# Kernel optimization log

Hardware: AMD Instinct MI355X
Metric: run time of the kernel (lower is better)

Reference implementation:

```python
import jax, jax.numpy as jnp
import numpy as np

VOCAB, EMB, HID, OUT = 32000, 512, 1024, 2
B, T = 64, 512


def setup_inputs() -> dict:
    key = jax.random.key(0)
    ks = jax.random.split(key, 12)
    def xavier(k, shape):
        fan_in, fan_out = shape
        lim = np.sqrt(6.0 / (fan_in + fan_out)).astype(np.float32)
        return jax.random.uniform(k, shape, jnp.float32, -lim, lim)
    x = jax.random.randint(ks[0], (B, T), 0, VOCAB, dtype=jnp.int32)
    emb = jax.random.uniform(ks[1], (VOCAB, EMB), jnp.float32, -0.1, 0.1)
    inp = {
        "x": x,
        "emb": emb,
        "Wxi": xavier(ks[2], (EMB, HID)), "Whi": xavier(ks[3], (HID, HID)), "bi": jnp.zeros((HID,), jnp.float32),
        "Wxf": xavier(ks[4], (EMB, HID)), "Whf": xavier(ks[5], (HID, HID)), "bf": jnp.zeros((HID,), jnp.float32),
        "Wxc": xavier(ks[6], (EMB, HID)), "Whc": xavier(ks[7], (HID, HID)), "bc": jnp.zeros((HID,), jnp.float32),
        "Wxo": xavier(ks[8], (EMB, HID)), "Who": xavier(ks[9], (HID, HID)), "bo": jnp.zeros((HID,), jnp.float32),
        "Why": xavier(ks[10], (HID, OUT)), "by": jnp.zeros((OUT,), jnp.float32),
    }
    return inp


def reference(x, emb, Wxi, Whi, bi, Wxf, Whf, bf, Wxc, Whc, bc, Wxo, Who, bo, Why, by):
    # Embedding lookup: [B, T, E]
    xe = emb[x]
    # Precompute input projections for all 4 gates in one batched contraction each.
    # Stack Wx matrices -> [E, 4H]; gates_x: [T, B, 4H] (time-major for scan)
    Wx = jnp.concatenate([Wxi, Wxf, Wxc, Wxo], axis=1)          # [E, 4H]
    Wh = jnp.concatenate([Whi, Whf, Whc, Who], axis=1)          # [H, 4H]
    b = jnp.concatenate([bi, bf, bc, bo], axis=0)               # [4H]
    gates_x = jnp.einsum('bte,eg->tbg', xe, Wx)                  # [T, B, 4H]
    H = Whi.shape[0]

    def step(carry, gx):
        h, c = carry
        g = gx + h @ Wh + b                                      # [B, 4H]
        i = jax.nn.sigmoid(g[:, 0 * H:1 * H])
        f = jax.nn.sigmoid(g[:, 1 * H:2 * H])
        gg = jnp.tanh(g[:, 2 * H:3 * H])
        o = jax.nn.sigmoid(g[:, 3 * H:4 * H])
        c = f * c + i * gg
        h = o * jnp.tanh(c)
        return (h, c), None

    h0 = jnp.zeros((x.shape[0], H), xe.dtype)
    c0 = jnp.zeros((x.shape[0], H), xe.dtype)
    (h, c), _ = jax.lax.scan(step, (h0, c0), gates_x)
    # dropout is identity in eval mode
    return h @ Why + by
```

## Files before the change

### kernel.cpp

```cpp
#include <hip/hip_runtime.h>

#define TT 512
#define BB 64
#define EMB 512
#define HID 1024
#define K4 1536
#define NBLK 256
#define THREADS 512

typedef __bf16 bf16x8 __attribute__((ext_vector_type(8)));
typedef float f32x4 __attribute__((ext_vector_type(4)));

__device__ __forceinline__ unsigned short f2bf(float f) {
    union { float f; unsigned u; } v; v.f = f;
    unsigned u = v.u;
    unsigned r = u + 0x7FFFu + ((u >> 16) & 1u);
    return (unsigned short)(r >> 16);
}

__global__ void zero_kernel(unsigned* p, int n) {
    int i = blockIdx.x * 256 + threadIdx.x;
    if (i < n) p[i] = 0u;
}

__global__ void xe_kernel(const int* __restrict__ x, const float* __restrict__ emb,
                          unsigned short* __restrict__ xe_all) {
    int rowid = blockIdx.x;
    int t = rowid >> 6, b = rowid & 63;
    int idx = x[b * TT + t];
    float4 v = ((const float4*)(emb + (long)idx * EMB))[threadIdx.x];
    ushort4 o;
    o.x = f2bf(v.x); o.y = f2bf(v.y); o.z = f2bf(v.z); o.w = f2bf(v.w);
    ((ushort4*)(xe_all + (long)rowid * EMB))[threadIdx.x] = o;
}

__global__ void wpack_kernel(const float* __restrict__ Wxi, const float* __restrict__ Whi,
                             const float* __restrict__ Wxf, const float* __restrict__ Whf,
                             const float* __restrict__ Wxc, const float* __restrict__ Whc,
                             const float* __restrict__ Wxo, const float* __restrict__ Who,
                             unsigned short* __restrict__ Wpack) {
    const float* Wx[4] = {Wxi, Wxf, Wxc, Wxo};
    const float* Wh[4] = {Whi, Whf, Whc, Who};
    int n0 = (blockIdx.x & 15) << 8;
    int k0 = (blockIdx.x >> 4) << 3;
    int g = n0 >> 10, col0 = n0 & 1023;
    const float* base = (k0 < 512) ? (Wx[g] + (long)k0 * HID + col0)
                                   : (Wh[g] + (long)(k0 - 512) * HID + col0);
    int tid = threadIdx.x;
    union { unsigned short s[8]; uint4 v; } out;
#pragma unroll
    for (int i = 0; i < 8; ++i) out.s[i] = f2bf(base[(long)i * HID + tid]);
    *(uint4*)(Wpack + (long)(n0 + tid) * K4 + k0) = out.v;
}

#define MFMA(a, b, c) __builtin_amdgcn_mfma_f32_16x16x32_bf16((a), (b), (c), 0, 0, 0)

__launch_bounds__(THREADS, 2)
__global__ void lstm_kernel(const unsigned short* __restrict__ xe_all,
                            const unsigned short* __restrict__ Wpack,
                            unsigned short* __restrict__ hbuf,
                            float* __restrict__ hfinal,
                            unsigned* __restrict__ arrive,
                            const float* __restrict__ bi_p, const float* __restrict__ bf_p,
                            const float* __restrict__ bc_p, const float* __restrict__ bo_p) {
    __shared__ unsigned short Wlds[32 * 1536];
    __shared__ __align__(16) float partials[4][32][44];

    const int tid = threadIdx.x;
    const int wave = tid >> 6, lane = tid & 63;
    const int quad = lane >> 4, r16 = lane & 15;
    const int ks4 = wave >> 1;
    const int mw = wave & 1;
    const int bid = blockIdx.x;
    const int half = bid & 1;
    const int pidx = bid >> 1;
    const int j0 = pidx * 8;

#pragma unroll
    for (int i = 0; i < 12; ++i) {
        int gidx = tid + i * THREADS;
        int c = gidx / 192, q = gidx % 192;
        int n = ((c >> 3) << 10) + j0 + (c & 7);
        *(uint4*)(&Wlds[(c * 192 + (q ^ (c & 7))) * 8]) =
            *(const uint4*)(Wpack + (long)n * K4 + q * 8);
    }
    const int b_loc = (tid & 255) >> 3, jj = tid & 7;
    const int b_ = half * 32 + b_loc;
    float rb0 = 0.f, rb1 = 0.f, rb2 = 0.f, rb3 = 0.f;
    if (tid < 256) {
        rb0 = bi_p[j0 + jj]; rb1 = bf_p[j0 + jj];
        rb2 = bc_p[j0 + jj]; rb3 = bo_p[j0 + jj];
    }
    float c_state = 0.f;
    __syncthreads();

    const f32x4 zf = {0.f, 0.f, 0.f, 0.f};
    const int row0 = half * 32 + mw * 16 + r16;
    const int s0 = r16 & 7;

    for (int t = 0; t < TT; ++t) {
        const unsigned short* xe_t = xe_all + (long)t * (BB * EMB);
        const unsigned short* hb = hbuf + (t & 1) * (BB * HID);

        f32x4 acc0 = zf, acc1 = zf;

        {
            uint4 xa[4];
#pragma unroll
            for (int i = 0; i < 4; ++i) {
                int k = ks4 * 128 + i * 32 + quad * 8;
                xa[i] = *(const uint4*)(xe_t + (long)row0 * EMB + k);
            }
#pragma unroll
            for (int i = 0; i < 4; ++i) {
                int bk = (ks4 * 128 + i * 32 + quad * 8) >> 3;
                bf16x8 b0 = *(const bf16x8*)(&Wlds[(r16 * 192 + (bk ^ s0)) * 8]);
                bf16x8 b1 = *(const bf16x8*)(&Wlds[((16 + r16) * 192 + (bk ^ s0)) * 8]);
                bf16x8 a0 = __builtin_bit_cast(bf16x8, xa[i]);
                acc0 = MFMA(a0, b0, acc0); acc1 = MFMA(a0, b1, acc1);
            }
        }

        if (t > 0) {
            const unsigned* fp = &arrive[((t - 1) * 16 + half * 8 + ks4 * 2 + (lane & 1)) * 16];
            while (!__all(__hip_atomic_load(fp, __ATOMIC_RELAXED,
                                            __HIP_MEMORY_SCOPE_AGENT) >= 16u))
                __builtin_amdgcn_s_sleep(1);
            asm volatile("" ::: "memory");
        }

        {
            uint4 ha[8];
#pragma unroll
            for (int i = 0; i < 8; ++i) {
                const unsigned short* p0 = hb + (long)row0 * HID + ks4 * 256 + i * 32 + quad * 8;
                asm volatile("global_load_dwordx4 %0, %1, off sc1" : "=v"(ha[i]) : "v"(p0));
            }
            asm volatile("s_waitcnt vmcnt(0)" ::: "memory");
#pragma unroll
            for (int i = 0; i < 8; ++i) {
                int bk = (512 + ks4 * 256 + i * 32 + quad * 8) >> 3;
                bf16x8 b0 = *(const bf16x8*)(&Wlds[(r16 * 192 + (bk ^ s0)) * 8]);
                bf16x8 b1 = *(const bf16x8*)(&Wlds[((16 + r16) * 192 + (bk ^ s0)) * 8]);
                bf16x8 a0 = __builtin_bit_cast(bf16x8, ha[i]);
                acc0 = MFMA(a0, b0, acc0); acc1 = MFMA(a0, b1, acc1);
            }
        }

        {
            int pm = mw * 16 + quad * 4;
            *(f32x4*)&partials[ks4][r16][pm]      = acc0;
            *(f32x4*)&partials[ks4][16 + r16][pm] = acc1;
        }
        __syncthreads();

        if (tid < 256) {
            float gi = 0.f, gf = 0.f, gc = 0.f, go = 0.f;
#pragma unroll
            for (int w = 0; w < 4; ++w) {
                gi += partials[w][jj][b_loc];
                gf += partials[w][8 + jj][b_loc];
                gc += partials[w][16 + jj][b_loc];
                go += partials[w][24 + jj][b_loc];
            }
            gi += rb0; gf += rb1; gc += rb2; go += rb3;
            float si = 1.f / (1.f + __expf(-gi));
            float sf = 1.f / (1.f + __expf(-gf));
            float so = 1.f / (1.f + __expf(-go));
            float e2 = __expf(2.f * gc); float tc = (e2 - 1.f) / (e2 + 1.f);
            float c = sf * c_state + si * tc;
            c_state = c;
            float e2c = __expf(2.f * c); float th = (e2c - 1.f) / (e2c + 1.f);
            float h = so * th;
            unsigned short hv = f2bf(h);
            const unsigned short* hop = hbuf + ((t + 1) & 1) * (BB * HID) + b_ * HID + j0 + jj;
            asm volatile("global_store_short %0, %1, off sc1" :: "v"(hop), "v"(hv) : "memory");
            if (t == TT - 1) hfinal[b_ * HID + j0 + jj] = h;
        }
        asm volatile("s_waitcnt vmcnt(0)" ::: "memory");
        __syncthreads();
        if (tid == 0)
            __hip_atomic_fetch_add(&arrive[(t * 16 + half * 8 + (pidx >> 4)) * 16], 1u,
                                   __ATOMIC_RELAXED, __HIP_MEMORY_SCOPE_AGENT);
    }
}

__global__ void out_kernel(const float* __restrict__ hfinal, const float* __restrict__ Why,
                           const float* __restrict__ by, float* __restrict__ y) {
    int gw = blockIdx.x * 4 + (threadIdx.x >> 6);
    int lane = threadIdx.x & 63;
    int b = gw >> 1, o = gw & 1;
    float s = 0.f;
    for (int k = lane; k < HID; k += 64) s += hfinal[b * HID + k] * Why[k * 2 + o];
#pragma unroll
    for (int off = 32; off; off >>= 1) s += __shfl_down(s, off);
    if (lane == 0) y[b * 2 + o] = s + by[o];
}

extern "C" void kernel_launch(void* const* d_in, const int* in_sizes, int n_in,
                              void* d_out, int out_size, void* d_ws, size_t ws_size,
                              hipStream_t stream) {
    const int*   x   = (const int*)d_in[0];
    const float* emb = (const float*)d_in[1];
    const float* Wxi = (const float*)d_in[2];
    const float* Whi = (const float*)d_in[3];
    const float* bi  = (const float*)d_in[4];
    const float* Wxf = (const float*)d_in[5];
    const float* Whf = (const float*)d_in[6];
    const float* bfp = (const float*)d_in[7];
    const float* Wxc = (const float*)d_in[8];
    const float* Whc = (const float*)d_in[9];
    const float* bc  = (const float*)d_in[10];
    const float* Wxo = (const float*)d_in[11];
    const float* Who = (const float*)d_in[12];
    const float* bo  = (const float*)d_in[13];
    const float* Why = (const float*)d_in[14];
    const float* by  = (const float*)d_in[15];
    float* y = (float*)d_out;

    char* ws = (char*)d_ws;
    unsigned short* Wpack  = (unsigned short*)ws;
    unsigned short* xe_all = (unsigned short*)(ws + 12582912);
    unsigned short* hbuf   = (unsigned short*)(ws + 12582912 + 33554432);
    unsigned*       arrive = (unsigned*)(ws + 12582912 + 33554432 + 262144);
    float*          hfinal = (float*)(ws + 12582912 + 33554432 + 262144 + 524288);

    zero_kernel<<<768, 256, 0, stream>>>((unsigned*)hbuf, 196608);
    wpack_kernel<<<3072, 256, 0, stream>>>(Wxi, Whi, Wxf, Whf, Wxc, Whc, Wxo, Who, Wpack);
    xe_kernel<<<32768, 128, 0, stream>>>(x, emb, xe_all);

    const unsigned short* xe_p = xe_all;
    const unsigned short* Wp_p = Wpack;
    unsigned short* hb_p = hbuf;
    float* hf_p = hfinal;
    unsigned* ar_p = arrive;
    void* args[] = {&xe_p, &Wp_p, &hb_p, &hf_p, &ar_p,
                    (void*)&bi, (void*)&bfp, (void*)&bc, (void*)&bo};
    hipLaunchCooperativeKernel((void*)lstm_kernel, dim3(NBLK), dim3(THREADS), args, 0, stream);

    out_kernel<<<32, 256, 0, stream>>>(hfinal, Why, by, y);
}
```

Before: 2.412 ms.

## Replace arrival counters with step-tagged hidden-state words for inter-block sync

Each hidden value is now stored as a 32-bit word whose upper half holds the step index and lower half holds the bf16 value. Consumers poll the h data directly until every tag matches, which removes the separate atomic arrive counters, the global store drain and the extra block barrier. __syncthreads is also replaced with an LDS-only wait plus s_barrier. In exchange each step reads twice as many bytes of h, does more unpacking work and spins on data loads rather than on a single flag.

```diff
diff --git a/kernel.cpp b/kernel.cpp
--- a/kernel.cpp
+++ b/kernel.cpp
@@ -54,13 +54,22 @@
 }
 
 #define MFMA(a, b, c) __builtin_amdgcn_mfma_f32_16x16x32_bf16((a), (b), (c), 0, 0, 0)
+#define LDS_BARRIER() asm volatile("s_waitcnt lgkmcnt(0)\n\ts_barrier" ::: "memory")
+
+__device__ __forceinline__ bf16x8 unpack8(const uint4& lo, const uint4& hi) {
+    union { unsigned short s[8]; bf16x8 v; } u;
+    u.s[0] = (unsigned short)lo.x; u.s[1] = (unsigned short)lo.y;
+    u.s[2] = (unsigned short)lo.z; u.s[3] = (unsigned short)lo.w;
+    u.s[4] = (unsigned short)hi.x; u.s[5] = (unsigned short)hi.y;
+    u.s[6] = (unsigned short)hi.z; u.s[7] = (unsigned short)hi.w;
+    return u.v;
+}
 
 __launch_bounds__(THREADS, 2)
 __global__ void lstm_kernel(const unsigned short* __restrict__ xe_all,
                             const unsigned short* __restrict__ Wpack,
-                            unsigned short* __restrict__ hbuf,
+                            unsigned* __restrict__ hbuf2,
                             float* __restrict__ hfinal,
-                            unsigned* __restrict__ arrive,
                             const float* __restrict__ bi_p, const float* __restrict__ bf_p,
                             const float* __restrict__ bc_p, const float* __restrict__ bo_p) {
     __shared__ unsigned short Wlds[32 * 1536];
@@ -100,7 +109,6 @@
 
     for (int t = 0; t < TT; ++t) {
         const unsigned short* xe_t = xe_all + (long)t * (BB * EMB);
-        const unsigned short* hb = hbuf + (t & 1) * (BB * HID);
 
         f32x4 acc0 = zf, acc1 = zf;
 
@@ -121,28 +129,38 @@
             }
         }
 
-        if (t > 0) {
-            const unsigned* fp = &arrive[((t - 1) * 16 + half * 8 + ks4 * 2 + (lane & 1)) * 16];
-            while (!__all(__hip_atomic_load(fp, __ATOMIC_RELAXED,
-                                            __HIP_MEMORY_SCOPE_AGENT) >= 16u))
+        {
+            const unsigned* hrow = hbuf2 + (t & 1) * (BB * HID) + (long)row0 * HID + ks4 * 256;
+            uint4 ha[8][2];
+            const unsigned key = (unsigned)t << 16;
+            for (;;) {
+#pragma unroll
+                for (int i = 0; i < 8; ++i) {
+                    const unsigned* p0 = hrow + i * 32 + quad * 8;
+                    asm volatile("global_load_dwordx4 %0, %1, off sc1" : "=v"(ha[i][0]) : "v"(p0));
+                    asm volatile("global_load_dwordx4 %0, %1, off sc1" : "=v"(ha[i][1]) : "v"(p0 + 4));
+                }
+                asm volatile("s_waitcnt vmcnt(0)" ::: "memory");
+                unsigned bad = 0u;
+#pragma unroll
+                for (int i = 0; i < 8; ++i) {
+#pragma unroll
+                    for (int hgrp = 0; hgrp < 2; ++hgrp) {
+                        bad |= (ha[i][hgrp].x ^ key);
+                        bad |= (ha[i][hgrp].y ^ key);
+                        bad |= (ha[i][hgrp].z ^ key);
+                        bad |= (ha[i][hgrp].w ^ key);
+                    }
+                }
+                if (__all((bad & 0xFFFF0000u) == 0u)) break;
                 __builtin_amdgcn_s_sleep(1);
-            asm volatile("" ::: "memory");
-        }
-
-        {
-            uint4 ha[8];
-#pragma unroll
-            for (int i = 0; i < 8; ++i) {
-                const unsigned short* p0 = hb + (long)row0 * HID + ks4 * 256 + i * 32 + quad * 8;
-                asm volatile("global_load_dwordx4 %0, %1, off sc1" : "=v"(ha[i]) : "v"(p0));
-            }
-            asm volatile("s_waitcnt vmcnt(0)" ::: "memory");
+            }
 #pragma unroll
             for (int i = 0; i < 8; ++i) {
                 int bk = (512 + ks4 * 256 + i * 32 + quad * 8) >> 3;
                 bf16x8 b0 = *(const bf16x8*)(&Wlds[(r16 * 192 + (bk ^ s0)) * 8]);
                 bf16x8 b1 = *(const bf16x8*)(&Wlds[((16 + r16) * 192 + (bk ^ s0)) * 8]);
-                bf16x8 a0 = __builtin_bit_cast(bf16x8, ha[i]);
+                bf16x8 a0 = unpack8(ha[i][0], ha[i][1]);
                 acc0 = MFMA(a0, b0, acc0); acc1 = MFMA(a0, b1, acc1);
             }
         }
@@ -152,7 +170,7 @@
             *(f32x4*)&partials[ks4][r16][pm]      = acc0;
             *(f32x4*)&partials[ks4][16 + r16][pm] = acc1;
         }
-        __syncthreads();
+        LDS_BARRIER();
 
         if (tid < 256) {
             float gi = 0.f, gf = 0.f, gc = 0.f, go = 0.f;
@@ -172,16 +190,12 @@
             c_state = c;
             float e2c = __expf(2.f * c); float th = (e2c - 1.f) / (e2c + 1.f);
             float h = so * th;
-            unsigned short hv = f2bf(h);
-            const unsigned short* hop = hbuf + ((t + 1) & 1) * (BB * HID) + b_ * HID + j0 + jj;
-            asm volatile("global_store_short %0, %1, off sc1" :: "v"(hop), "v"(hv) : "memory");
+            unsigned word = ((unsigned)(t + 1) << 16) | (unsigned)f2bf(h);
+            unsigned* hop = hbuf2 + ((t + 1) & 1) * (BB * HID) + b_ * HID + j0 + jj;
+            asm volatile("global_store_dword %0, %1, off sc1" :: "v"(hop), "v"(word) : "memory");
             if (t == TT - 1) hfinal[b_ * HID + j0 + jj] = h;
         }
-        asm volatile("s_waitcnt vmcnt(0)" ::: "memory");
-        __syncthreads();
-        if (tid == 0)
-            __hip_atomic_fetch_add(&arrive[(t * 16 + half * 8 + (pidx >> 4)) * 16], 1u,
-                                   __ATOMIC_RELAXED, __HIP_MEMORY_SCOPE_AGENT);
+        LDS_BARRIER();
     }
 }
 
@@ -221,20 +235,18 @@
     char* ws = (char*)d_ws;
     unsigned short* Wpack  = (unsigned short*)ws;
     unsigned short* xe_all = (unsigned short*)(ws + 12582912);
-    unsigned short* hbuf   = (unsigned short*)(ws + 12582912 + 33554432);
-    unsigned*       arrive = (unsigned*)(ws + 12582912 + 33554432 + 262144);
-    float*          hfinal = (float*)(ws + 12582912 + 33554432 + 262144 + 524288);
-
-    zero_kernel<<<768, 256, 0, stream>>>((unsigned*)hbuf, 196608);
+    unsigned*       hbuf2  = (unsigned*)(ws + 12582912 + 33554432);
+    float*          hfinal = (float*)(ws + 12582912 + 33554432 + 524288);
+
+    zero_kernel<<<512, 256, 0, stream>>>(hbuf2, 131072);
     wpack_kernel<<<3072, 256, 0, stream>>>(Wxi, Whi, Wxf, Whf, Wxc, Whc, Wxo, Who, Wpack);
     xe_kernel<<<32768, 128, 0, stream>>>(x, emb, xe_all);
 
     const unsigned short* xe_p = xe_all;
     const unsigned short* Wp_p = Wpack;
-    unsigned short* hb_p = hbuf;
+    unsigned* hb_p = hbuf2;
     float* hf_p = hfinal;
-    unsigned* ar_p = arrive;
-    void* args[] = {&xe_p, &Wp_p, &hb_p, &hf_p, &ar_p,
+    void* args[] = {&xe_p, &Wp_p, &hb_p, &hf_p,
                     (void*)&bi, (void*)&bfp, (void*)&bc, (void*)&bo};
     hipLaunchCooperativeKernel((void*)lstm_kernel, dim3(NBLK), dim3(THREADS), args, 0, stream);
 
```

After: 5.055 ms. 110% more time.
